# Performance work log

Measured on AMD Instinct MI355X. Metric: run time of the kernel, lower is better.

Reference implementation:

```python
import jax, jax.numpy as jnp
import numpy as np

B, S, E, H = 4, 512, 64, 1024


def setup_inputs() -> dict:
    key = jax.random.key(0)
    k1, k2, k3 = jax.random.split(key, 3)
    cell_states = jax.random.normal(k1, (B, S, E, H), dtype=jnp.float32)
    # stacked per-entity Linear(hidden, 1) weights and biases
    W = jax.random.normal(k2, (E, H), dtype=jnp.float32) * (1.0 / np.sqrt(H))
    b = jax.random.normal(k3, (E,), dtype=jnp.float32) * 0.01
    return {"cell_states": cell_states, "W": W, "b": b}


def reference(cell_states, W, b):
    # Fused form of the per-entity Linear loop:
    # out[b, s, e] = sum_h cell_states[b, s, e, h] * W[e, h] + b[e]
    return jnp.einsum("bseh,eh->bse", cell_states, W) + b
```

## Files before the change

### kernel.cpp

```cpp
#include <hip/hip_runtime.h>
#include <hip/hip_bf16.h>


#define H_DIM 1024
#define E_DIM 64

__global__ __launch_bounds__(256) void Cell_to_Entity_78735340470739_kernel(
    const float* __restrict__ x,
    const float* __restrict__ W,
    const float* __restrict__ bias,
    float* __restrict__ out,
    int n_out)
{
    const int wave_in_block = threadIdx.x >> 6;
    const int lane          = threadIdx.x & 63;
    const int o = blockIdx.x * (blockDim.x >> 6) + wave_in_block;
    if (o >= n_out) return;

    const int e = o & (E_DIM - 1);

    const float4* __restrict__ xp = (const float4*)(x + (size_t)o * H_DIM);
    const float4* __restrict__ wp = (const float4*)(W + (size_t)e * H_DIM);

    float acc = 0.0f;
#pragma unroll
    for (int k = 0; k < 4; ++k) {
        const float4 xv = xp[lane + k * 64];
        const float4 wv = wp[lane + k * 64];
        acc += xv.x * wv.x + xv.y * wv.y + xv.z * wv.z + xv.w * wv.w;
    }

#pragma unroll
    for (int off = 32; off > 0; off >>= 1)
        acc += __shfl_down(acc, off, 64);

    if (lane == 0)
        out[o] = acc + bias[e];
}

extern "C" void kernel_launch(void* const* d_in, const int* in_sizes, int n_in,
                              void* d_out, int out_size, void* d_ws, size_t ws_size,
                              hipStream_t stream) {
    const float* x    = (const float*)d_in[0];
    const float* W    = (const float*)d_in[1];
    const float* bias = (const float*)d_in[2];
    float* out        = (float*)d_out;

    const int n_out = out_size;
    const int waves_per_block = 4;
    const int blocks = (n_out + waves_per_block - 1) / waves_per_block;

    Cell_to_Entity_78735340470739_kernel<<<blocks, 256, 0, stream>>>(
        x, W, bias, out, n_out);
}
```

Baseline: 661.4 us.

## Use persistent grid-stride waves with register-cached weights and nontemporal loads

```diff
diff --git a/kernel.cpp b/kernel.cpp
--- a/kernel.cpp
+++ b/kernel.cpp
@@ -4,6 +4,8 @@
 
 #define H_DIM 1024
 #define E_DIM 64
+
+typedef float v4f __attribute__((ext_vector_type(4)));
 
 __global__ __launch_bounds__(256) void Cell_to_Entity_78735340470739_kernel(
     const float* __restrict__ x,
@@ -12,30 +14,74 @@
     float* __restrict__ out,
     int n_out)
 {
-    const int wave_in_block = threadIdx.x >> 6;
-    const int lane          = threadIdx.x & 63;
-    const int o = blockIdx.x * (blockDim.x >> 6) + wave_in_block;
-    if (o >= n_out) return;
+    const int lane    = threadIdx.x & 63;
+    const int wave    = (int)((blockIdx.x * blockDim.x + threadIdx.x) >> 6);
+    const int n_waves = (int)((gridDim.x * blockDim.x) >> 6);
 
-    const int e = o & (E_DIM - 1);
+    const int e           = wave & (E_DIM - 1);
+    const int waves_per_e = n_waves >> 6;
+    const int r0          = wave >> 6;
+    const int R           = n_out >> 6;
 
-    const float4* __restrict__ xp = (const float4*)(x + (size_t)o * H_DIM);
-    const float4* __restrict__ wp = (const float4*)(W + (size_t)e * H_DIM);
+    const v4f* __restrict__ wp = (const v4f*)(W + (size_t)e * H_DIM);
+    const v4f w0 = wp[lane];
+    const v4f w1 = wp[lane + 64];
+    const v4f w2 = wp[lane + 128];
+    const v4f w3 = wp[lane + 192];
+    const float be = bias[e];
 
-    float acc = 0.0f;
-#pragma unroll
-    for (int k = 0; k < 4; ++k) {
-        const float4 xv = xp[lane + k * 64];
-        const float4 wv = wp[lane + k * 64];
-        acc += xv.x * wv.x + xv.y * wv.y + xv.z * wv.z + xv.w * wv.w;
-    }
+    int r = r0;
+    for (; r + waves_per_e < R; r += 2 * waves_per_e) {
+        const int oa = r * E_DIM + e;
+        const int ob = (r + waves_per_e) * E_DIM + e;
+        const v4f* __restrict__ xa = (const v4f*)(x + (size_t)oa * H_DIM);
+        const v4f* __restrict__ xb = (const v4f*)(x + (size_t)ob * H_DIM);
+
+        const v4f a0 = __builtin_nontemporal_load(&xa[lane]);
+        const v4f a1 = __builtin_nontemporal_load(&xa[lane + 64]);
+        const v4f a2 = __builtin_nontemporal_load(&xa[lane + 128]);
+        const v4f a3 = __builtin_nontemporal_load(&xa[lane + 192]);
+        const v4f b0 = __builtin_nontemporal_load(&xb[lane]);
+        const v4f b1 = __builtin_nontemporal_load(&xb[lane + 64]);
+        const v4f b2 = __builtin_nontemporal_load(&xb[lane + 128]);
+        const v4f b3 = __builtin_nontemporal_load(&xb[lane + 192]);
+
+        float acc_a = a0.x*w0.x + a0.y*w0.y + a0.z*w0.z + a0.w*w0.w
+                    + a1.x*w1.x + a1.y*w1.y + a1.z*w1.z + a1.w*w1.w
+                    + a2.x*w2.x + a2.y*w2.y + a2.z*w2.z + a2.w*w2.w
+                    + a3.x*w3.x + a3.y*w3.y + a3.z*w3.z + a3.w*w3.w;
+        float acc_b = b0.x*w0.x + b0.y*w0.y + b0.z*w0.z + b0.w*w0.w
+                    + b1.x*w1.x + b1.y*w1.y + b1.z*w1.z + b1.w*w1.w
+                    + b2.x*w2.x + b2.y*w2.y + b2.z*w2.z + b2.w*w2.w
+                    + b3.x*w3.x + b3.y*w3.y + b3.z*w3.z + b3.w*w3.w;
 
 #pragma unroll
-    for (int off = 32; off > 0; off >>= 1)
-        acc += __shfl_down(acc, off, 64);
-
-    if (lane == 0)
-        out[o] = acc + bias[e];
+        for (int off = 32; off > 0; off >>= 1) {
+            acc_a += __shfl_down(acc_a, off, 64);
+            acc_b += __shfl_down(acc_b, off, 64);
+        }
+        if (lane == 0) {
+            out[oa] = acc_a + be;
+            out[ob] = acc_b + be;
+        }
+    }
+    for (; r < R; r += waves_per_e) {
+        const int o = r * E_DIM + e;
+        const v4f* __restrict__ xp = (const v4f*)(x + (size_t)o * H_DIM);
+        const v4f a0 = __builtin_nontemporal_load(&xp[lane]);
+        const v4f a1 = __builtin_nontemporal_load(&xp[lane + 64]);
+        const v4f a2 = __builtin_nontemporal_load(&xp[lane + 128]);
+        const v4f a3 = __builtin_nontemporal_load(&xp[lane + 192]);
+        float acc = a0.x*w0.x + a0.y*w0.y + a0.z*w0.z + a0.w*w0.w
+                  + a1.x*w1.x + a1.y*w1.y + a1.z*w1.z + a1.w*w1.w
+                  + a2.x*w2.x + a2.y*w2.y + a2.z*w2.z + a2.w*w2.w
+                  + a3.x*w3.x + a3.y*w3.y + a3.z*w3.z + a3.w*w3.w;
+#pragma unroll
+        for (int off = 32; off > 0; off >>= 1)
+            acc += __shfl_down(acc, off, 64);
+        if (lane == 0)
+            out[o] = acc + be;
+    }
 }
 
 extern "C" void kernel_launch(void* const* d_in, const int* in_sizes, int n_in,
@@ -47,9 +93,7 @@
     float* out        = (float*)d_out;
 
     const int n_out = out_size;
-    const int waves_per_block = 4;
-    const int blocks = (n_out + waves_per_block - 1) / waves_per_block;
-
+    const int blocks = 2048;
     Cell_to_Entity_78735340470739_kernel<<<blocks, 256, 0, stream>>>(
         x, W, bias, out, n_out);
 }
```

New measurement: 644.9 us. 1.03x faster.
